# Performance work log

Measured on AMD Instinct MI355X. Metric: run time of the kernel, lower is better.

Reference implementation:

```python
import jax, jax.numpy as jnp
import numpy as np

B, S, HID, NH = 4, 1024, 1024, 16
DK = HID // NH
SCALE = DK ** -0.5
NEG = -9e15


def setup_inputs() -> dict:
    key = jax.random.key(0)
    ks = jax.random.split(key, 10)
    std = HID ** -0.5
    return {
        "batch": jax.random.normal(ks[0], (B, S, HID), jnp.float32),
        "attn_bias": jax.random.normal(ks[1], (B, NH, S, S), jnp.float32),
        "Wq": jax.random.normal(ks[2], (HID, HID), jnp.float32) * std,
        "bq": jnp.zeros((HID,), jnp.float32),
        "Wk": jax.random.normal(ks[3], (HID, HID), jnp.float32) * std,
        "bk": jnp.zeros((HID,), jnp.float32),
        "Wv": jax.random.normal(ks[4], (HID, HID), jnp.float32) * std,
        "bv": jnp.zeros((HID,), jnp.float32),
        "Wo": jax.random.normal(ks[5], (HID, HID), jnp.float32) * std,
        "bo": jnp.zeros((HID,), jnp.float32),
    }


def reference(batch, attn_bias, Wq, bq, Wk, bk, Wv, bv, Wo, bo):
    b, s, _ = batch.shape
    # QKV projections -> [b, h, s, d]
    q = (batch @ Wq.T + bq).reshape(b, s, NH, DK).transpose(0, 2, 1, 3)
    k = (batch @ Wk.T + bk).reshape(b, s, NH, DK).transpose(0, 2, 1, 3)
    v = (batch @ Wv.T + bv).reshape(b, s, NH, DK).transpose(0, 2, 1, 3)
    # scaled scores [b, h, s, s]
    x = jnp.einsum("bhqd,bhkd->bhqk", q * SCALE, k)
    # custom zero-mask: exact zeros become -9e15
    x = jnp.where(x == 0, jnp.float32(NEG), x)
    x = x + attn_bias
    p = jax.nn.softmax(x, axis=3)  # dropout_rate=0.0 -> identity
    o = jnp.einsum("bhqk,bhkd->bhqd", p, v)
    o = o.transpose(0, 2, 1, 3).reshape(b, s, NH * DK)
    return o @ Wo.T + bo
```

## Files before the change

### kernel.cpp

```cpp
#include <hip/hip_runtime.h>
#include <hip/hip_bf16.h>
#include <stdint.h>
#include <stddef.h>

#define Bd  4
#define Sd  1024
#define Hd  1024
#define NHd 16
#define DKd 64
#define SCALEF 0.125f
#define NEGV  -9.0e15f
#define L2E   1.4426950408889634f

typedef __attribute__((ext_vector_type(8))) short bfrag;
typedef __attribute__((ext_vector_type(4))) float facc;
typedef __attribute__((ext_vector_type(4))) float f32x4;

typedef __attribute__((address_space(1))) const unsigned int ga_u32;
typedef __attribute__((address_space(3))) unsigned int ls_u32;

__device__ __forceinline__ void gload_lds16(const void* g, void* l) {
  __builtin_amdgcn_global_load_lds((ga_u32*)g, (ls_u32*)l, 16, 0, 0);
}

__device__ __forceinline__ unsigned short f2bf(float f) {
  unsigned int u = __float_as_uint(f);
  u += 0x7fffu + ((u >> 16) & 1u);
  return (unsigned short)(u >> 16);
}

__global__ void castk_all(const float* __restrict__ s0, const float* __restrict__ s1,
                          const float* __restrict__ s2, const float* __restrict__ s3,
                          const float* __restrict__ s4,
                          unsigned short* __restrict__ d0, unsigned short* __restrict__ d1,
                          unsigned short* __restrict__ d2, unsigned short* __restrict__ d3,
                          unsigned short* __restrict__ d4) {
  const int id = blockIdx.x;
  const float* s; unsigned short* d; int i;
  if (id < 4096) { s = s0; d = d0; i = id * 256 + threadIdx.x; }
  else {
    const int w = (id - 4096) >> 10;
    s = (w == 0) ? s1 : (w == 1) ? s2 : (w == 2) ? s3 : s4;
    d = (w == 0) ? d1 : (w == 1) ? d2 : (w == 2) ? d3 : d4;
    i = ((id - 4096) & 1023) * 256 + threadIdx.x;
  }
  float4 v = ((const float4*)s)[i];
  ushort4 ov;
  ov.x = f2bf(v.x); ov.y = f2bf(v.y); ov.z = f2bf(v.z); ov.w = f2bf(v.w);
  ((ushort4*)d)[i] = ov;
}

__global__ __launch_bounds__(256, 3)
void gemm_qkv(const unsigned short* __restrict__ A,
              const unsigned short* __restrict__ W0, const unsigned short* __restrict__ W1,
              const unsigned short* __restrict__ W2,
              const float* __restrict__ b0, const float* __restrict__ b1, const float* __restrict__ b2,
              unsigned short* __restrict__ o0, unsigned short* __restrict__ o1, unsigned short* __restrict__ o2) {
  __shared__ __align__(16) unsigned short smem[128 * 136];
  unsigned short* sA = smem;
  unsigned short* sB = smem + 4096;
  const int z = blockIdx.z;
  const unsigned short* Bm = (z == 0) ? W0 : (z == 1) ? W1 : W2;
  const float* bias = (z == 0) ? b0 : (z == 1) ? b1 : b2;
  unsigned short* out = (z == 0) ? o0 : (z == 1) ? o1 : o2;

  const int m0 = blockIdx.x * 128, n0 = blockIdx.y * 128;
  const int tid = threadIdx.x;
  const int wave = tid >> 6, lane = tid & 63;
  const int quad = lane >> 4, l16 = lane & 15;
  const int wm = wave >> 1, wn = wave & 1;

  facc acc[4][4] = {};

  const int j0 = wave * 128 + lane;
  const int j1 = j0 + 64;
  const int row0 = j0 >> 2, ko0 = (j0 & 3) << 3;
  const int row1 = j1 >> 2, ko1 = (j1 & 3) << 3;
  const size_t aoff0 = (size_t)(m0 + row0) * 1024 + ko0;
  const size_t aoff1 = (size_t)(m0 + row1) * 1024 + ko1;
  const size_t boff0 = (size_t)(n0 + row0) * 1024 + ko0;
  const size_t boff1 = (size_t)(n0 + row1) * 1024 + ko1;
  unsigned short* sA0 = sA + (wave * 2 + 0) * 512;
  unsigned short* sA1 = sA + (wave * 2 + 1) * 512;
  unsigned short* sB0 = sB + (wave * 2 + 0) * 512;
  unsigned short* sB1 = sB + (wave * 2 + 1) * 512;

  for (int k0 = 0; k0 < 1024; k0 += 32) {
    gload_lds16(A + aoff0 + k0, sA0);
    gload_lds16(A + aoff1 + k0, sA1);
    gload_lds16(Bm + boff0 + k0, sB0);
    gload_lds16(Bm + boff1 + k0, sB1);
    __syncthreads();
    bfrag af[4], bf[4];
#pragma unroll
    for (int i = 0; i < 4; ++i) af[i] = *(const bfrag*)(sA + (wm * 64 + i * 16 + l16) * 32 + quad * 8);
#pragma unroll
    for (int j = 0; j < 4; ++j) bf[j] = *(const bfrag*)(sB + (wn * 64 + j * 16 + l16) * 32 + quad * 8);
#pragma unroll
    for (int i = 0; i < 4; ++i)
#pragma unroll
      for (int j = 0; j < 4; ++j)
        acc[i][j] = __builtin_amdgcn_mfma_f32_16x16x32_bf16(af[i], bf[j], acc[i][j], 0, 0, 0);
    __syncthreads();
  }

  if (z < 2) {
#pragma unroll
    for (int i = 0; i < 4; ++i)
#pragma unroll
      for (int j = 0; j < 4; ++j) {
        const int col = n0 + wn * 64 + j * 16 + l16;
        const float bv = bias[col];
        const int h = col >> 6, d = col & 63;
#pragma unroll
        for (int r = 0; r < 4; ++r) {
          const int m = m0 + wm * 64 + i * 16 + quad * 4 + r;
          const int b = m >> 10, s = m & 1023;
          out[(((size_t)(b * NHd + h) * Sd) + s) * DKd + d] = f2bf(acc[i][j][r] + bv);
        }
      }
  } else {
    unsigned short* sT = smem;
#pragma unroll
    for (int i = 0; i < 4; ++i)
#pragma unroll
      for (int j = 0; j < 4; ++j) {
        const int col = n0 + wn * 64 + j * 16 + l16;
        const float bv = bias[col];
        const int nrow = wn * 64 + j * 16 + l16;
        const int mbase = wm * 64 + i * 16 + quad * 4;
        ushort4 pk;
        pk.x = f2bf(acc[i][j][0] + bv);
        pk.y = f2bf(acc[i][j][1] + bv);
        pk.z = f2bf(acc[i][j][2] + bv);
        pk.w = f2bf(acc[i][j][3] + bv);
        *(ushort4*)(sT + nrow * 136 + mbase) = pk;
      }
    __syncthreads();
    const int bI = m0 >> 10, s0i = m0 & 1023;
#pragma unroll
    for (int it = 0; it < 8; ++it) {
      const int c = tid + it * 256;
      const int row = c >> 4, mc = (c & 15) * 8;
      bfrag vv = *(const bfrag*)(sT + row * 136 + mc);
      const int col = n0 + row, hh = col >> 6, dd = col & 63;
      *(bfrag*)(out + (((size_t)(bI * NHd + hh) * DKd) + dd) * Sd + s0i + mc) = vv;
    }
  }
}

__global__ __launch_bounds__(256, 3)
void gemm_out(const unsigned short* __restrict__ A, const unsigned short* __restrict__ Bm,
              const float* __restrict__ bias, float* __restrict__ out) {
  __shared__ __align__(16) unsigned short sA[64 * 64];
  __shared__ __align__(16) unsigned short sB[128 * 64];
  const int m0 = blockIdx.x * 64, n0 = blockIdx.y * 128;
  const int tid = threadIdx.x;
  const int wave = tid >> 6, lane = tid & 63;
  const int quad = lane >> 4, l16 = lane & 15;

  facc acc[8] = {};

  const int cA0 = (wave * 2 + 0) * 64 + lane;
  const int cA1 = (wave * 2 + 1) * 64 + lane;
  const int rA0 = cA0 >> 3, kA0 = ((cA0 & 7) ^ (rA0 & 7)) * 8;
  const int rA1 = cA1 >> 3, kA1 = ((cA1 & 7) ^ (rA1 & 7)) * 8;
  const size_t aoff0 = (size_t)(m0 + rA0) * 1024 + kA0;
  const size_t aoff1 = (size_t)(m0 + rA1) * 1024 + kA1;
  size_t boff[4];
#pragma unroll
  for (int i = 0; i < 4; ++i) {
    const int c = (wave * 4 + i) * 64 + lane;
    const int r = c >> 3, kk = ((c & 7) ^ (r & 7)) * 8;
    boff[i] = (size_t)(n0 + r) * 1024 + kk;
  }

  for (int k0 = 0; k0 < 1024; k0 += 64) {
    gload_lds16(A + aoff0 + k0, sA + (wave * 2 + 0) * 512);
    gload_lds16(A + aoff1 + k0, sA + (wave * 2 + 1) * 512);
#pragma unroll
    for (int i = 0; i < 4; ++i)
      gload_lds16(Bm + boff[i] + k0, sB + (wave * 4 + i) * 512);
    __syncthreads();
#pragma unroll
    for (int c2 = 0; c2 < 2; ++c2) {
      const int ko = ((c2 * 4 + quad) ^ (l16 & 7)) * 8;
      bfrag af = *(const bfrag*)(sA + (wave * 16 + l16) * 64 + ko);
#pragma unroll
      for (int j = 0; j < 8; ++j) {
        bfrag bf = *(const bfrag*)(sB + (j * 16 + l16) * 64 + ko);
        acc[j] = __builtin_amdgcn_mfma_f32_16x16x32_bf16(af, bf, acc[j], 0, 0, 0);
      }
    }
    __syncthreads();
  }

#pragma unroll
  for (int j = 0; j < 8; ++j) {
    const int col = n0 + j * 16 + l16;
    const float bv = bias[col];
#pragma unroll
    for (int r = 0; r < 4; ++r) {
      const int m = m0 + wave * 16 + quad * 4 + r;
      out[(size_t)m * 1024 + col] = acc[j][r] + bv;
    }
  }
}

__global__ __attribute__((amdgpu_flat_work_group_size(128, 128), amdgpu_waves_per_eu(4, 4)))
void attn_kernel(const unsigned short* __restrict__ q,
                 const unsigned short* __restrict__ k,
                 const unsigned short* __restrict__ vt,
                 const float* __restrict__ bias,
                 unsigned short* __restrict__ o)
{
  __shared__ __align__(16) float sS[2][16][132];
  const int p = blockIdx.x;
  const int xcd = p & 7;
  const int g = p >> 3;
  const int bh = ((g >> 5) << 3) | xcd;
  const int q0 = (g & 31) * 32;
  const int tid = threadIdx.x;
  const int wave = tid >> 6, lane = tid & 63;
  const int quad = lane >> 4, l16 = lane & 15;
  const int b = bh >> 4, h = bh & 15;

  const unsigned short* qh = q + (size_t)bh * Sd * DKd;
  const unsigned short* kh = k + (size_t)bh * Sd * DKd;
  const unsigned short* vh = vt + (size_t)bh * DKd * Sd;
  const float* bias_h = bias + (size_t)bh * Sd * Sd;
  const int rq = q0 + wave * 16;
  float (*sSw)[132] = sS[wave];

  bfrag qf[2];
#pragma unroll
  for (int c = 0; c < 2; ++c)
    qf[c] = *(const bfrag*)(qh + (size_t)(rq + l16) * DKd + c * 32 + quad * 8);

  facc oacc[4] = {};
  float lsum = 0.f;
  const float SL2 = SCALEF * L2E;

  const float* bp = bias_h + (size_t)(rq + l16) * Sd + quad * 8;
  f32x4 br[8];
#pragma unroll
  for (int c = 0; c < 4; ++c) {
    br[2 * c]     = __builtin_nontemporal_load((const f32x4*)(bp + c * 32));
    br[2 * c + 1] = __builtin_nontemporal_load((const f32x4*)(bp + c * 32 + 4));
  }

  for (int t = 0; t < 8; ++t) {
    const int k0 = t * 128;
    facc sacc[8] = {};
#pragma unroll
    for (int c = 0; c < 2; ++c)
#pragma unroll
      for (int j = 0; j < 8; ++j) {
        bfrag kf = *(const bfrag*)(kh + (size_t)(k0 + j * 16 + l16) * DKd + c * 32 + quad * 8);
        sacc[j] = __builtin_amdgcn_mfma_f32_16x16x32_bf16(qf[c], kf, sacc[j], 0, 0, 0);
      }
#pragma unroll
    for (int j = 0; j < 8; ++j)
#pragma unroll
      for (int r = 0; r < 4; ++r)
        sSw[quad * 4 + r][j * 16 + l16] = sacc[j][r];
#pragma unroll
    for (int c = 0; c < 4; ++c) {
      const float* sp = &sSw[l16][quad * 8 + c * 32];
      const f32x4 s0 = *(const f32x4*)sp;
      const f32x4 s1 = *(const f32x4*)(sp + 4);
      const f32x4 b0 = br[2 * c], b1 = br[2 * c + 1];
      float e0 = exp2f(fmaf(s0.x, SL2, b0.x * L2E)); e0 = (s0.x == 0.f) ? 0.f : e0;
      float e1 = exp2f(fmaf(s0.y, SL2, b0.y * L2E)); e1 = (s0.y == 0.f) ? 0.f : e1;
      float e2 = exp2f(fmaf(s0.z, SL2, b0.z * L2E)); e2 = (s0.z == 0.f) ? 0.f : e2;
      float e3 = exp2f(fmaf(s0.w, SL2, b0.w * L2E)); e3 = (s0.w == 0.f) ? 0.f : e3;
      float e4 = exp2f(fmaf(s1.x, SL2, b1.x * L2E)); e4 = (s1.x == 0.f) ? 0.f : e4;
      float e5 = exp2f(fmaf(s1.y, SL2, b1.y * L2E)); e5 = (s1.y == 0.f) ? 0.f : e5;
      float e6 = exp2f(fmaf(s1.z, SL2, b1.z * L2E)); e6 = (s1.z == 0.f) ? 0.f : e6;
      float e7 = exp2f(fmaf(s1.w, SL2, b1.w * L2E)); e7 = (s1.w == 0.f) ? 0.f : e7;
      lsum += ((e0 + e1) + (e2 + e3)) + ((e4 + e5) + (e6 + e7));
      bfrag pf;
      pf[0] = (short)f2bf(e0); pf[1] = (short)f2bf(e1);
      pf[2] = (short)f2bf(e2); pf[3] = (short)f2bf(e3);
      pf[4] = (short)f2bf(e4); pf[5] = (short)f2bf(e5);
      pf[6] = (short)f2bf(e6); pf[7] = (short)f2bf(e7);
#pragma unroll
      for (int n = 0; n < 4; ++n) {
        bfrag vf = *(const bfrag*)(vh + (size_t)(n * 16 + l16) * Sd + k0 + c * 32 + quad * 8);
        oacc[n] = __builtin_amdgcn_mfma_f32_16x16x32_bf16(pf, vf, oacc[n], 0, 0, 0);
      }
    }
    if (t < 7) {
      const float* bpn = bp + k0 + 128;
#pragma unroll
      for (int c = 0; c < 4; ++c) {
        br[2 * c]     = __builtin_nontemporal_load((const f32x4*)(bpn + c * 32));
        br[2 * c + 1] = __builtin_nontemporal_load((const f32x4*)(bpn + c * 32 + 4));
      }
    }
  }

  lsum += __shfl_xor(lsum, 16, 64);
  lsum += __shfl_xor(lsum, 32, 64);

#pragma unroll
  for (int r = 0; r < 4; ++r) {
    const float rs = __shfl(lsum, quad * 4 + r, 64);
    const float rinv = 1.0f / rs;
    const size_t rowo = (size_t)(b * Sd + rq + quad * 4 + r) * Hd + h * 64;
#pragma unroll
    for (int n = 0; n < 4; ++n)
      o[rowo + n * 16 + l16] = f2bf(oacc[n][r] * rinv);
  }
}

extern "C" void kernel_launch(void* const* d_in, const int* in_sizes, int n_in,
                              void* d_out, int out_size, void* d_ws, size_t ws_size,
                              hipStream_t stream) {
  const float* batch = (const float*)d_in[0];
  const float* attn_bias = (const float*)d_in[1];
  const float* Wq = (const float*)d_in[2];
  const float* bq = (const float*)d_in[3];
  const float* Wk = (const float*)d_in[4];
  const float* bk = (const float*)d_in[5];
  const float* Wv = (const float*)d_in[6];
  const float* bv = (const float*)d_in[7];
  const float* Wo = (const float*)d_in[8];
  const float* bo = (const float*)d_in[9];
  float* out = (float*)d_out;

  unsigned short* ws = (unsigned short*)d_ws;
  unsigned short* Ab  = ws;
  unsigned short* Wqb = Ab  + 4194304;
  unsigned short* Wkb = Wqb + 1048576;
  unsigned short* Wvb = Wkb + 1048576;
  unsigned short* Wob = Wvb + 1048576;
  unsigned short* qb  = Wob + 1048576;
  unsigned short* kb  = qb  + 4194304;
  unsigned short* vtb = kb  + 4194304;
  unsigned short* ob  = vtb + 4194304;

  castk_all<<<8192, 256, 0, stream>>>(batch, Wq, Wk, Wv, Wo, Ab, Wqb, Wkb, Wvb, Wob);
  gemm_qkv<<<dim3(32, 8, 3), 256, 0, stream>>>(Ab, Wqb, Wkb, Wvb, bq, bk, bv, qb, kb, vtb);
  attn_kernel<<<dim3(2048), 128, 0, stream>>>(qb, kb, vtb, attn_bias, ob);
  gemm_out<<<dim3(64, 8), 256, 0, stream>>>(ob, Wob, bo, out);
}
```

Measured before the change: 535.6 us.

## Transpose attention MFMAs so scores land per-query-row, shrinking LDS staging to bf16 P

Swaps the MFMA operand order (K·Q and V·P) so each lane holds four consecutive key columns of one query row. Softmax then runs directly on accumulator registers, and only packed bf16 probabilities go through a small LDS tile instead of the full fp32 score tile. The key tile shrinks from 128 to 64 per iteration with matching bias prefetch, and the fast exp2 intrinsic is used. The output is written as 4-wide vector stores and the row-sum shuffle broadcast is removed. In exchange the loop has twice as many iterations with smaller MFMA batches per step.

```diff
diff --git a/kernel.cpp b/kernel.cpp
--- a/kernel.cpp
+++ b/kernel.cpp
@@ -214,7 +214,7 @@
                  const float* __restrict__ bias,
                  unsigned short* __restrict__ o)
 {
-  __shared__ __align__(16) float sS[2][16][132];
+  __shared__ __align__(16) unsigned int sP[2][16][36];
   const int p = blockIdx.x;
   const int xcd = p & 7;
   const int g = p >> 3;
@@ -230,7 +230,7 @@
   const unsigned short* vh = vt + (size_t)bh * DKd * Sd;
   const float* bias_h = bias + (size_t)bh * Sd * Sd;
   const int rq = q0 + wave * 16;
-  float (*sSw)[132] = sS[wave];
+  unsigned int (*sPw)[36] = sP[wave];
 
   bfrag qf[2];
 #pragma unroll
@@ -241,76 +241,75 @@
   float lsum = 0.f;
   const float SL2 = SCALEF * L2E;
 
-  const float* bp = bias_h + (size_t)(rq + l16) * Sd + quad * 8;
-  f32x4 br[8];
-#pragma unroll
-  for (int c = 0; c < 4; ++c) {
-    br[2 * c]     = __builtin_nontemporal_load((const f32x4*)(bp + c * 32));
-    br[2 * c + 1] = __builtin_nontemporal_load((const f32x4*)(bp + c * 32 + 4));
-  }
-
-  for (int t = 0; t < 8; ++t) {
-    const int k0 = t * 128;
-    facc sacc[8] = {};
+  const float* bpS = bias_h + (size_t)(rq + l16) * Sd + quad * 4;
+  f32x4 br0 = __builtin_nontemporal_load((const f32x4*)(bpS + 0));
+  f32x4 br1 = __builtin_nontemporal_load((const f32x4*)(bpS + 16));
+  f32x4 br2 = __builtin_nontemporal_load((const f32x4*)(bpS + 32));
+  f32x4 br3 = __builtin_nontemporal_load((const f32x4*)(bpS + 48));
+
+  for (int t = 0; t < 16; ++t) {
+    const int k0 = t * 64;
+    facc sacc[4] = {};
 #pragma unroll
     for (int c = 0; c < 2; ++c)
 #pragma unroll
-      for (int j = 0; j < 8; ++j) {
+      for (int j = 0; j < 4; ++j) {
         bfrag kf = *(const bfrag*)(kh + (size_t)(k0 + j * 16 + l16) * DKd + c * 32 + quad * 8);
-        sacc[j] = __builtin_amdgcn_mfma_f32_16x16x32_bf16(qf[c], kf, sacc[j], 0, 0, 0);
-      }
-#pragma unroll
-    for (int j = 0; j < 8; ++j)
-#pragma unroll
-      for (int r = 0; r < 4; ++r)
-        sSw[quad * 4 + r][j * 16 + l16] = sacc[j][r];
-#pragma unroll
-    for (int c = 0; c < 4; ++c) {
-      const float* sp = &sSw[l16][quad * 8 + c * 32];
-      const f32x4 s0 = *(const f32x4*)sp;
-      const f32x4 s1 = *(const f32x4*)(sp + 4);
-      const f32x4 b0 = br[2 * c], b1 = br[2 * c + 1];
-      float e0 = exp2f(fmaf(s0.x, SL2, b0.x * L2E)); e0 = (s0.x == 0.f) ? 0.f : e0;
-      float e1 = exp2f(fmaf(s0.y, SL2, b0.y * L2E)); e1 = (s0.y == 0.f) ? 0.f : e1;
-      float e2 = exp2f(fmaf(s0.z, SL2, b0.z * L2E)); e2 = (s0.z == 0.f) ? 0.f : e2;
-      float e3 = exp2f(fmaf(s0.w, SL2, b0.w * L2E)); e3 = (s0.w == 0.f) ? 0.f : e3;
-      float e4 = exp2f(fmaf(s1.x, SL2, b1.x * L2E)); e4 = (s1.x == 0.f) ? 0.f : e4;
-      float e5 = exp2f(fmaf(s1.y, SL2, b1.y * L2E)); e5 = (s1.y == 0.f) ? 0.f : e5;
-      float e6 = exp2f(fmaf(s1.z, SL2, b1.z * L2E)); e6 = (s1.z == 0.f) ? 0.f : e6;
-      float e7 = exp2f(fmaf(s1.w, SL2, b1.w * L2E)); e7 = (s1.w == 0.f) ? 0.f : e7;
-      lsum += ((e0 + e1) + (e2 + e3)) + ((e4 + e5) + (e6 + e7));
-      bfrag pf;
-      pf[0] = (short)f2bf(e0); pf[1] = (short)f2bf(e1);
-      pf[2] = (short)f2bf(e2); pf[3] = (short)f2bf(e3);
-      pf[4] = (short)f2bf(e4); pf[5] = (short)f2bf(e5);
-      pf[6] = (short)f2bf(e6); pf[7] = (short)f2bf(e7);
+        sacc[j] = __builtin_amdgcn_mfma_f32_16x16x32_bf16(kf, qf[c], sacc[j], 0, 0, 0);
+      }
+    asm volatile("" : "+v"(br0), "+v"(br1), "+v"(br2), "+v"(br3));
+    unsigned int pk[4][2];
+#pragma unroll
+    for (int j = 0; j < 4; ++j) {
+      const f32x4 bb = (j == 0) ? br0 : (j == 1) ? br1 : (j == 2) ? br2 : br3;
+      float e0 = __builtin_amdgcn_exp2f(fmaf(sacc[j][0], SL2, bb.x * L2E));
+      float e1 = __builtin_amdgcn_exp2f(fmaf(sacc[j][1], SL2, bb.y * L2E));
+      float e2 = __builtin_amdgcn_exp2f(fmaf(sacc[j][2], SL2, bb.z * L2E));
+      float e3 = __builtin_amdgcn_exp2f(fmaf(sacc[j][3], SL2, bb.w * L2E));
+      e0 = (sacc[j][0] == 0.f) ? 0.f : e0;
+      e1 = (sacc[j][1] == 0.f) ? 0.f : e1;
+      e2 = (sacc[j][2] == 0.f) ? 0.f : e2;
+      e3 = (sacc[j][3] == 0.f) ? 0.f : e3;
+      lsum += (e0 + e1) + (e2 + e3);
+      pk[j][0] = (unsigned int)f2bf(e0) | ((unsigned int)f2bf(e1) << 16);
+      pk[j][1] = (unsigned int)f2bf(e2) | ((unsigned int)f2bf(e3) << 16);
+    }
+    if (t < 15) {
+      const float* bpn = bpS + k0 + 64;
+      br0 = __builtin_nontemporal_load((const f32x4*)(bpn + 0));
+      br1 = __builtin_nontemporal_load((const f32x4*)(bpn + 16));
+      br2 = __builtin_nontemporal_load((const f32x4*)(bpn + 32));
+      br3 = __builtin_nontemporal_load((const f32x4*)(bpn + 48));
+    }
+#pragma unroll
+    for (int j = 0; j < 4; ++j) {
+      uint2 w; w.x = pk[j][0]; w.y = pk[j][1];
+      *(uint2*)&sPw[l16][j * 8 + quad * 2] = w;
+    }
+#pragma unroll
+    for (int c = 0; c < 2; ++c) {
+      bfrag pf = *(const bfrag*)&sPw[l16][c * 16 + quad * 4];
 #pragma unroll
       for (int n = 0; n < 4; ++n) {
         bfrag vf = *(const bfrag*)(vh + (size_t)(n * 16 + l16) * Sd + k0 + c * 32 + quad * 8);
-        oacc[n] = __builtin_amdgcn_mfma_f32_16x16x32_bf16(pf, vf, oacc[n], 0, 0, 0);
-      }
-    }
-    if (t < 7) {
-      const float* bpn = bp + k0 + 128;
-#pragma unroll
-      for (int c = 0; c < 4; ++c) {
-        br[2 * c]     = __builtin_nontemporal_load((const f32x4*)(bpn + c * 32));
-        br[2 * c + 1] = __builtin_nontemporal_load((const f32x4*)(bpn + c * 32 + 4));
+        oacc[n] = __builtin_amdgcn_mfma_f32_16x16x32_bf16(vf, pf, oacc[n], 0, 0, 0);
       }
     }
   }
 
   lsum += __shfl_xor(lsum, 16, 64);
   lsum += __shfl_xor(lsum, 32, 64);
-
-#pragma unroll
-  for (int r = 0; r < 4; ++r) {
-    const float rs = __shfl(lsum, quad * 4 + r, 64);
-    const float rinv = 1.0f / rs;
-    const size_t rowo = (size_t)(b * Sd + rq + quad * 4 + r) * Hd + h * 64;
-#pragma unroll
-    for (int n = 0; n < 4; ++n)
-      o[rowo + n * 16 + l16] = f2bf(oacc[n][r] * rinv);
+  const float rinv = 1.0f / lsum;
+
+  const size_t rowo = (size_t)(b * Sd + rq + l16) * Hd + h * 64 + quad * 4;
+#pragma unroll
+  for (int n = 0; n < 4; ++n) {
+    ushort4 st;
+    st.x = f2bf(oacc[n][0] * rinv);
+    st.y = f2bf(oacc[n][1] * rinv);
+    st.z = f2bf(oacc[n][2] * rinv);
+    st.w = f2bf(oacc[n][3] * rinv);
+    *(ushort4*)(o + rowo + n * 16) = st;
   }
 }
 
```

New measurement: 536.7 us. About the same (+0.2%).
